# Performance work log

Hardware: AMD Instinct MI355X
Metric: run time of the kernel (lower is better)

Reference implementation:

```python
import jax, jax.numpy as jnp
import numpy as np

B, T, E = 4096, 200, 64
H1, H2 = 80, 40  # att_hidden_units


def setup_inputs() -> dict:
    key = jax.random.key(0)
    ks = jax.random.split(key, 9)
    glorot = jax.nn.initializers.glorot_normal()
    return {
        "queries": jax.random.normal(ks[0], (B, 1, E), jnp.float32),
        "keys": jax.random.normal(ks[1], (B, T, E), jnp.float32),
        "keys_length": jax.random.randint(ks[2], (B, 1), 0, T, jnp.int32),
        "W1": glorot(ks[3], (2 * E, H1), jnp.float32),
        "b1": jnp.zeros((H1,), jnp.float32),
        "W2": glorot(ks[4], (H1, H2), jnp.float32),
        "b2": jnp.zeros((H2,), jnp.float32),
        "kernel": glorot(ks[5], (H2, 1), jnp.float32),
        "bias": jnp.zeros((1,), jnp.float32),
    }


def reference(queries, keys, keys_length, W1, b1, W2, b2, kernel, bias):
    b, t, e = keys.shape
    # tile query across all T key positions and concat -> (B, T, 2E)
    q = jnp.broadcast_to(queries, (b, t, e))
    att_input = jnp.concatenate([q, keys], axis=-1)
    # local activation unit: small per-key MLP with sigmoid activations
    h = jax.nn.sigmoid(att_input @ W1 + b1)   # (B, T, H1)
    h = jax.nn.sigmoid(h @ W2 + b2)           # (B, T, H2)
    score = h @ kernel + bias                 # (B, T, 1)
    scores = jnp.transpose(score, (0, 2, 1))  # (B, 1, T)
    # sequence mask from keys_length (B, 1)
    mask = jnp.arange(t)[None, None, :] < keys_length[:, :, None]  # (B, 1, T)
    paddings = jnp.full_like(scores, -(2.0 ** 32) + 1.0)
    scores = jnp.where(mask, scores, paddings)
    # weight_normalization=True -> softmax over T
    weights = jax.nn.softmax(scores, axis=-1)  # (B, 1, T)
    # weighted-sum pooling over keys -> (B, 1, E)
    out = jnp.matmul(weights, keys)
    return out
```

## Files before the change

### kernel.cpp

```cpp
#include <hip/hip_runtime.h>
#include <hip/hip_bf16.h>

#define TT 200
#define EE 64

typedef unsigned short u16;
typedef unsigned int u32;
typedef __attribute__((ext_vector_type(8))) short bfrag;
typedef __attribute__((ext_vector_type(4))) float f32x4;

__device__ __forceinline__ u16 f2bf(float f) {
    __hip_bfloat16 h(f);
    return __builtin_bit_cast(u16, h);
}
__device__ __forceinline__ float bf2f(u16 h) {
    return __uint_as_float(((u32)h) << 16);
}
__device__ __forceinline__ float sigmoid_fast(float x) {
    return __builtin_amdgcn_rcpf(1.0f + __expf(-x));
}

__global__ void prep_frags(const float* __restrict__ W1, const float* __restrict__ W2,
                           u16* __restrict__ A1p, u16* __restrict__ A2p,
                           u16* __restrict__ A1q) {
    int idx = blockIdx.x * 256 + threadIdx.x;
    if (idx < 5 * 2 * 64 * 8) {
        int j = idx & 7, l = (idx >> 3) & 63, ks = (idx >> 9) & 1, mt5 = idx >> 10;
        int g = l >> 4, m = mt5 * 16 + (l & 15);
        int k = ks * 32 + g * 8 + j;
        A1p[idx] = f2bf(W1[(64 + k) * 80 + m]);
        A1q[idx] = f2bf(W1[k * 80 + m]);
    }
    if (idx < 3 * 3 * 64 * 8) {
        int j = idx & 7, l = (idx >> 3) & 63, ks = (idx >> 9) % 3, m2 = idx / 1536;
        int g = l >> 4, m = m2 * 16 + (l & 15);
        int i24 = ks * 8 + j;
        u16 v = 0;
        if (i24 < 20 && m < 40) {
            int mt5 = i24 >> 2, r = i24 & 3;
            int k = mt5 * 16 + g * 4 + r;
            v = f2bf(W2[k * 40 + m]);
        }
        A2p[idx] = v;
    }
}

#define LOADK32(MT, QA0, QA1, QA2, QA3, QB0, QB1, QB2, QB3) {           \
    int ra_ = (MT) * 32 + l15;                                          \
    QA0 = QA1 = QA2 = QA3 = make_float4(0.f, 0.f, 0.f, 0.f);            \
    QB0 = QB1 = QB2 = QB3 = make_float4(0.f, 0.f, 0.f, 0.f);            \
    if (ra_ < lenEff) {                                                 \
        const float* p_ = kb + ra_ * EE + g * 8;                        \
        QA0 = *reinterpret_cast<const float4*>(p_);                     \
        QA1 = *reinterpret_cast<const float4*>(p_ + 4);                 \
        QA2 = *reinterpret_cast<const float4*>(p_ + 32);                \
        QA3 = *reinterpret_cast<const float4*>(p_ + 36);                \
    }                                                                   \
    if (ra_ + 16 < lenEff) {                                            \
        const float* p_ = kb + (ra_ + 16) * EE + g * 8;                 \
        QB0 = *reinterpret_cast<const float4*>(p_);                     \
        QB1 = *reinterpret_cast<const float4*>(p_ + 4);                 \
        QB2 = *reinterpret_cast<const float4*>(p_ + 32);                \
        QB3 = *reinterpret_cast<const float4*>(p_ + 36);                \
    } }

#define PACK(A, X, Y) {                                                 \
    A[0] = (short)f2bf(X.x); A[1] = (short)f2bf(X.y);                   \
    A[2] = (short)f2bf(X.z); A[3] = (short)f2bf(X.w);                   \
    A[4] = (short)f2bf(Y.x); A[5] = (short)f2bf(Y.y);                   \
    A[6] = (short)f2bf(Y.z); A[7] = (short)f2bf(Y.w); }

__global__ __launch_bounds__(256, 2) void din_mfma(
    const float* __restrict__ queries,
    const float* __restrict__ keys,
    const int*   __restrict__ keys_length,
    const float* __restrict__ b1,
    const float* __restrict__ b2,
    const float* __restrict__ wk,
    const float* __restrict__ bias,
    const u16*   __restrict__ A1p,
    const u16*   __restrict__ A2p,
    const u16*   __restrict__ A1q,
    float* __restrict__ out)
{
    __shared__ __align__(16) u16 w1ls[5 * 2 * 64 * 8];
    __shared__ __align__(16) u16 w2ls[3 * 3 * 64 * 8];
    __shared__ __align__(16) float wkls[48];
    __shared__ __align__(16) float b2ls[48];
    __shared__ __align__(16) float qils[4][80];

    const int tid  = threadIdx.x;
    const int lane = tid & 63;
    const int wv   = tid >> 6;
    const int l15  = lane & 15;
    const int g    = lane >> 4;
    const int b    = blockIdx.x * 4 + wv;

    const float* kb = keys + (size_t)b * (TT * EE);
    const float* q  = queries + (size_t)b * EE;
    const int len   = keys_length[b];
    const float biass = bias[0];

    const int lenEff = (len == 0) ? TT : len;
    const int ntiles = (lenEff + 31) >> 5;

    float4 qa0, qa1, qa2, qa3, qb0, qb1_, qb2, qb3;
    LOADK32(0, qa0, qa1, qa2, qa3, qb0, qb1_, qb2, qb3);

    for (int c = tid; c < 640; c += 256)
        *reinterpret_cast<float4*>(&w1ls[c * 8]) = reinterpret_cast<const float4*>(A1p)[c];
    for (int c = tid; c < 576; c += 256)
        *reinterpret_cast<float4*>(&w2ls[c * 8]) = reinterpret_cast<const float4*>(A2p)[c];
    if (tid < 48) {
        wkls[tid] = (tid < 40) ? wk[tid] : 0.f;
        b2ls[tid] = (tid < 40) ? b2[tid] : 0.f;
    }

    {
        bfrag qf0, qf1;
        const float* qp = q + g * 8;
        float4 q0 = *reinterpret_cast<const float4*>(qp);
        float4 q1 = *reinterpret_cast<const float4*>(qp + 4);
        float4 q2 = *reinterpret_cast<const float4*>(qp + 32);
        float4 q3 = *reinterpret_cast<const float4*>(qp + 36);
        PACK(qf0, q0, q1); PACK(qf1, q2, q3);
        #pragma unroll
        for (int mt5 = 0; mt5 < 5; ++mt5) {
            bfrag aq0 = *reinterpret_cast<const bfrag*>(A1q + (((mt5 * 2 + 0) * 64 + lane) << 3));
            bfrag aq1 = *reinterpret_cast<const bfrag*>(A1q + (((mt5 * 2 + 1) * 64 + lane) << 3));
            f32x4 c = { 0.f, 0.f, 0.f, 0.f };
            c = __builtin_amdgcn_mfma_f32_16x16x32_bf16(aq0, qf0, c, 0, 0, 0);
            c = __builtin_amdgcn_mfma_f32_16x16x32_bf16(aq1, qf1, c, 0, 0, 0);
            float4 bv = *reinterpret_cast<const float4*>(b1 + mt5 * 16 + g * 4);
            if (l15 == 0) {
                float4 o = { c[0] + bv.x, c[1] + bv.y, c[2] + bv.z, c[3] + bv.w };
                *reinterpret_cast<float4*>(&qils[wv][mt5 * 16 + g * 4]) = o;
            }
        }
    }
    __syncthreads();

    float acc[16];
    #pragma unroll
    for (int j = 0; j < 16; ++j) acc[j] = 0.f;
    float Z = 0.f;

    bfrag a0, a1, a2, a3;
    PACK(a0, qa0, qa1); PACK(a1, qa2, qa3);
    PACK(a2, qb0, qb1_); PACK(a3, qb2, qb3);

    for (int mt = 0; mt < ntiles; ++mt) {
        if (mt + 1 < ntiles) { LOADK32(mt + 1, qa0, qa1, qa2, qa3, qb0, qb1_, qb2, qb3); }
        const bool hasB = (mt * 32 + 16) < lenEff;

        bfrag xa0, xa1, xa2;
        {
            f32x4 d[5];
            #pragma unroll
            for (int mt5 = 0; mt5 < 5; ++mt5) {
                bfrag wA = *reinterpret_cast<const bfrag*>(&w1ls[((mt5 * 2 + 0) * 64 + lane) * 8]);
                bfrag wB = *reinterpret_cast<const bfrag*>(&w1ls[((mt5 * 2 + 1) * 64 + lane) * 8]);
                f32x4 c = *reinterpret_cast<const f32x4*>(&qils[wv][mt5 * 16 + g * 4]);
                c = __builtin_amdgcn_mfma_f32_16x16x32_bf16(wA, a0, c, 0, 0, 0);
                c = __builtin_amdgcn_mfma_f32_16x16x32_bf16(wB, a1, c, 0, 0, 0);
                d[mt5] = c;
            }
            #pragma unroll
            for (int j = 0; j < 8; ++j) {
                xa0[j] = (short)f2bf(sigmoid_fast(d[j >> 2][j & 3]));
                xa1[j] = (short)f2bf(sigmoid_fast(d[(8 + j) >> 2][(8 + j) & 3]));
                xa2[j] = (short)((16 + j) < 20
                            ? f2bf(sigmoid_fast(d[(16 + j) >> 2][(16 + j) & 3])) : 0);
            }
        }

        float pa = 0.f, pb = 0.f, ea, eb;
        const int ra = mt * 32 + l15, rb = ra + 16;

        if (hasB) {
            bfrag xb0, xb1, xb2;
            {
                f32x4 d[5];
                #pragma unroll
                for (int mt5 = 0; mt5 < 5; ++mt5) {
                    bfrag wA = *reinterpret_cast<const bfrag*>(&w1ls[((mt5 * 2 + 0) * 64 + lane) * 8]);
                    bfrag wB = *reinterpret_cast<const bfrag*>(&w1ls[((mt5 * 2 + 1) * 64 + lane) * 8]);
                    f32x4 c = *reinterpret_cast<const f32x4*>(&qils[wv][mt5 * 16 + g * 4]);
                    c = __builtin_amdgcn_mfma_f32_16x16x32_bf16(wA, a2, c, 0, 0, 0);
                    c = __builtin_amdgcn_mfma_f32_16x16x32_bf16(wB, a3, c, 0, 0, 0);
                    d[mt5] = c;
                }
                #pragma unroll
                for (int j = 0; j < 8; ++j) {
                    xb0[j] = (short)f2bf(sigmoid_fast(d[j >> 2][j & 3]));
                    xb1[j] = (short)f2bf(sigmoid_fast(d[(8 + j) >> 2][(8 + j) & 3]));
                    xb2[j] = (short)((16 + j) < 20
                                ? f2bf(sigmoid_fast(d[(16 + j) >> 2][(16 + j) & 3])) : 0);
                }
            }
            #pragma unroll
            for (int m2 = 0; m2 < 3; ++m2) {
                bfrag u0 = *reinterpret_cast<const bfrag*>(&w2ls[((m2 * 3 + 0) * 64 + lane) * 8]);
                bfrag u1 = *reinterpret_cast<const bfrag*>(&w2ls[((m2 * 3 + 1) * 64 + lane) * 8]);
                bfrag u2 = *reinterpret_cast<const bfrag*>(&w2ls[((m2 * 3 + 2) * 64 + lane) * 8]);
                f32x4 ci = *reinterpret_cast<const f32x4*>(&b2ls[m2 * 16 + g * 4]);
                f32x4 wv4 = *reinterpret_cast<const f32x4*>(&wkls[m2 * 16 + g * 4]);
                f32x4 ca = ci, cb = ci;
                ca = __builtin_amdgcn_mfma_f32_16x16x32_bf16(u0, xa0, ca, 0, 0, 0);
                ca = __builtin_amdgcn_mfma_f32_16x16x32_bf16(u1, xa1, ca, 0, 0, 0);
                ca = __builtin_amdgcn_mfma_f32_16x16x32_bf16(u2, xa2, ca, 0, 0, 0);
                cb = __builtin_amdgcn_mfma_f32_16x16x32_bf16(u0, xb0, cb, 0, 0, 0);
                cb = __builtin_amdgcn_mfma_f32_16x16x32_bf16(u1, xb1, cb, 0, 0, 0);
                cb = __builtin_amdgcn_mfma_f32_16x16x32_bf16(u2, xb2, cb, 0, 0, 0);
                #pragma unroll
                for (int rr = 0; rr < 4; ++rr) {
                    pa = fmaf(sigmoid_fast(ca[rr]), wv4[rr], pa);
                    pb = fmaf(sigmoid_fast(cb[rr]), wv4[rr], pb);
                }
            }
            pa += __shfl_xor(pa, 16); pa += __shfl_xor(pa, 32);
            pb += __shfl_xor(pb, 16); pb += __shfl_xor(pb, 32);
            ea = (ra < len) ? __expf(pa + biass) : ((len == 0 && ra < TT) ? 1.f : 0.f);
            eb = (rb < len) ? __expf(pb + biass) : ((len == 0 && rb < TT) ? 1.f : 0.f);
            Z += ea + eb;
            #pragma unroll
            for (int j = 0; j < 8; ++j) {
                acc[j]     = fmaf(ea, bf2f((u16)a0[j]), fmaf(eb, bf2f((u16)a2[j]), acc[j]));
                acc[8 + j] = fmaf(ea, bf2f((u16)a1[j]), fmaf(eb, bf2f((u16)a3[j]), acc[8 + j]));
            }
        } else {
            #pragma unroll
            for (int m2 = 0; m2 < 3; ++m2) {
                bfrag u0 = *reinterpret_cast<const bfrag*>(&w2ls[((m2 * 3 + 0) * 64 + lane) * 8]);
                bfrag u1 = *reinterpret_cast<const bfrag*>(&w2ls[((m2 * 3 + 1) * 64 + lane) * 8]);
                bfrag u2 = *reinterpret_cast<const bfrag*>(&w2ls[((m2 * 3 + 2) * 64 + lane) * 8]);
                f32x4 ci = *reinterpret_cast<const f32x4*>(&b2ls[m2 * 16 + g * 4]);
                f32x4 wv4 = *reinterpret_cast<const f32x4*>(&wkls[m2 * 16 + g * 4]);
                f32x4 ca = ci;
                ca = __builtin_amdgcn_mfma_f32_16x16x32_bf16(u0, xa0, ca, 0, 0, 0);
                ca = __builtin_amdgcn_mfma_f32_16x16x32_bf16(u1, xa1, ca, 0, 0, 0);
                ca = __builtin_amdgcn_mfma_f32_16x16x32_bf16(u2, xa2, ca, 0, 0, 0);
                #pragma unroll
                for (int rr = 0; rr < 4; ++rr)
                    pa = fmaf(sigmoid_fast(ca[rr]), wv4[rr], pa);
            }
            pa += __shfl_xor(pa, 16); pa += __shfl_xor(pa, 32);
            ea = (ra < len) ? __expf(pa + biass) : ((len == 0 && ra < TT) ? 1.f : 0.f);
            Z += ea;
            #pragma unroll
            for (int j = 0; j < 8; ++j) {
                acc[j]     = fmaf(ea, bf2f((u16)a0[j]), acc[j]);
                acc[8 + j] = fmaf(ea, bf2f((u16)a1[j]), acc[8 + j]);
            }
        }

        if (mt + 1 < ntiles) {
            PACK(a0, qa0, qa1); PACK(a1, qa2, qa3);
            PACK(a2, qb0, qb1_); PACK(a3, qb2, qb3);
        }
    }

    Z += __shfl_xor(Z, 1); Z += __shfl_xor(Z, 2);
    Z += __shfl_xor(Z, 4); Z += __shfl_xor(Z, 8);
    #pragma unroll
    for (int j = 0; j < 16; ++j) {
        acc[j] += __shfl_xor(acc[j], 1);
        acc[j] += __shfl_xor(acc[j], 2);
        acc[j] += __shfl_xor(acc[j], 4);
        acc[j] += __shfl_xor(acc[j], 8);
    }
    if (l15 == 0) {
        float inv = __builtin_amdgcn_rcpf(Z);
        float* ob = out + (size_t)b * EE + g * 8;
        float4 o0 = { acc[0] * inv,  acc[1] * inv,  acc[2] * inv,  acc[3] * inv };
        float4 o1 = { acc[4] * inv,  acc[5] * inv,  acc[6] * inv,  acc[7] * inv };
        float4 o2 = { acc[8] * inv,  acc[9] * inv,  acc[10] * inv, acc[11] * inv };
        float4 o3 = { acc[12] * inv, acc[13] * inv, acc[14] * inv, acc[15] * inv };
        *reinterpret_cast<float4*>(ob)      = o0;
        *reinterpret_cast<float4*>(ob + 4)  = o1;
        *reinterpret_cast<float4*>(ob + 32) = o2;
        *reinterpret_cast<float4*>(ob + 36) = o3;
    }
}

extern "C" void kernel_launch(void* const* d_in, const int* in_sizes, int n_in,
                              void* d_out, int out_size, void* d_ws, size_t ws_size,
                              hipStream_t stream) {
    const float* queries = (const float*)d_in[0];
    const float* keys    = (const float*)d_in[1];
    const int*   klen    = (const int*)d_in[2];
    const float* W1      = (const float*)d_in[3];
    const float* b1      = (const float*)d_in[4];
    const float* W2      = (const float*)d_in[5];
    const float* b2      = (const float*)d_in[6];
    const float* wk      = (const float*)d_in[7];
    const float* bias    = (const float*)d_in[8];
    float* out           = (float*)d_out;

    u16* A1p = (u16*)d_ws;
    u16* A2p = (u16*)((char*)d_ws + 10240);
    u16* A1q = (u16*)((char*)d_ws + 19456);

    prep_frags<<<20, 256, 0, stream>>>(W1, W2, A1p, A2p, A1q);
    din_mfma<<<1024, 256, 0, stream>>>(queries, keys, klen, b1, b2, wk, bias,
                                       A1p, A2p, A1q, out);
}
```

Before: 51.66 us.

## Load-balance key tiles across the block's waves with an LDS work queue

Instead of each wave processing one batch row's tiles, all four waves in a block pull 32-row tiles from a shared atomic counter covering the block's four rows. Partial softmax numerators and denominators are written to LDS per wave and reduced at the end. This targets the imbalance caused by variable keys_length, where waves with short rows sit idle while one wave handles a long row. The cost is an LDS atomic per tile, extra LDS for the reduction buffers and a final block-wide sync. Because the shared exponentials are not max-subtracted, summing partials across waves is still exact.

```diff
diff --git a/kernel.cpp b/kernel.cpp
--- a/kernel.cpp
+++ b/kernel.cpp
@@ -45,23 +45,23 @@
     }
 }
 
-#define LOADK32(MT, QA0, QA1, QA2, QA3, QB0, QB1, QB2, QB3) {           \
-    int ra_ = (MT) * 32 + l15;                                          \
-    QA0 = QA1 = QA2 = QA3 = make_float4(0.f, 0.f, 0.f, 0.f);            \
-    QB0 = QB1 = QB2 = QB3 = make_float4(0.f, 0.f, 0.f, 0.f);            \
-    if (ra_ < lenEff) {                                                 \
-        const float* p_ = kb + ra_ * EE + g * 8;                        \
-        QA0 = *reinterpret_cast<const float4*>(p_);                     \
-        QA1 = *reinterpret_cast<const float4*>(p_ + 4);                 \
-        QA2 = *reinterpret_cast<const float4*>(p_ + 32);                \
-        QA3 = *reinterpret_cast<const float4*>(p_ + 36);                \
-    }                                                                   \
-    if (ra_ + 16 < lenEff) {                                            \
-        const float* p_ = kb + (ra_ + 16) * EE + g * 8;                 \
-        QB0 = *reinterpret_cast<const float4*>(p_);                     \
-        QB1 = *reinterpret_cast<const float4*>(p_ + 4);                 \
-        QB2 = *reinterpret_cast<const float4*>(p_ + 32);                \
-        QB3 = *reinterpret_cast<const float4*>(p_ + 36);                \
+#define LOADK32D(KB, MT, LEF, QA0, QA1, QA2, QA3, QB0, QB1, QB2, QB3) {  \
+    int ra_ = (MT) * 32 + l15;                                           \
+    QA0 = QA1 = QA2 = QA3 = make_float4(0.f, 0.f, 0.f, 0.f);             \
+    QB0 = QB1 = QB2 = QB3 = make_float4(0.f, 0.f, 0.f, 0.f);             \
+    if (ra_ < (LEF)) {                                                   \
+        const float* p_ = (KB) + ra_ * EE + g * 8;                       \
+        QA0 = *reinterpret_cast<const float4*>(p_);                      \
+        QA1 = *reinterpret_cast<const float4*>(p_ + 4);                  \
+        QA2 = *reinterpret_cast<const float4*>(p_ + 32);                 \
+        QA3 = *reinterpret_cast<const float4*>(p_ + 36);                 \
+    }                                                                    \
+    if (ra_ + 16 < (LEF)) {                                              \
+        const float* p_ = (KB) + (ra_ + 16) * EE + g * 8;                \
+        QB0 = *reinterpret_cast<const float4*>(p_);                      \
+        QB1 = *reinterpret_cast<const float4*>(p_ + 4);                  \
+        QB2 = *reinterpret_cast<const float4*>(p_ + 32);                 \
+        QB3 = *reinterpret_cast<const float4*>(p_ + 36);                 \
     } }
 
 #define PACK(A, X, Y) {                                                 \
@@ -88,24 +88,26 @@
     __shared__ __align__(16) float wkls[48];
     __shared__ __align__(16) float b2ls[48];
     __shared__ __align__(16) float qils[4][80];
+    __shared__ __align__(16) float redls[4][4][64];
+    __shared__ float zls[4][4];
+    __shared__ int ntls[4], lenls[4];
+    __shared__ u32 qh;
 
     const int tid  = threadIdx.x;
     const int lane = tid & 63;
     const int wv   = tid >> 6;
     const int l15  = lane & 15;
     const int g    = lane >> 4;
-    const int b    = blockIdx.x * 4 + wv;
-
-    const float* kb = keys + (size_t)b * (TT * EE);
-    const float* q  = queries + (size_t)b * EE;
-    const int len   = keys_length[b];
+    const int bbase = blockIdx.x * 4;
+    const int b    = bbase + wv;
     const float biass = bias[0];
 
-    const int lenEff = (len == 0) ? TT : len;
-    const int ntiles = (lenEff + 31) >> 5;
-
-    float4 qa0, qa1, qa2, qa3, qb0, qb1_, qb2, qb3;
-    LOADK32(0, qa0, qa1, qa2, qa3, qb0, qb1_, qb2, qb3);
+    const int len0 = keys_length[b];
+    const int lef0 = (len0 == 0) ? TT : len0;
+    if (lane == 0) { ntls[wv] = (lef0 + 31) >> 5; lenls[wv] = len0; }
+    if (tid == 0) qh = 0;
+    for (int c = tid; c < 1024; c += 256) (&redls[0][0][0])[c] = 0.f;
+    if (tid < 16) (&zls[0][0])[tid] = 0.f;
 
     for (int c = tid; c < 640; c += 256)
         *reinterpret_cast<float4*>(&w1ls[c * 8]) = reinterpret_cast<const float4*>(A1p)[c];
@@ -118,7 +120,7 @@
 
     {
         bfrag qf0, qf1;
-        const float* qp = q + g * 8;
+        const float* qp = queries + (size_t)b * EE + g * 8;
         float4 q0 = *reinterpret_cast<const float4*>(qp);
         float4 q1 = *reinterpret_cast<const float4*>(qp + 4);
         float4 q2 = *reinterpret_cast<const float4*>(qp + 32);
@@ -140,18 +142,47 @@
     }
     __syncthreads();
 
+    const int nt0 = ntls[0], nt1 = ntls[1], nt2 = ntls[2], nt3 = ntls[3];
+    const int c1 = nt0, c2 = nt0 + nt1, c3 = nt0 + nt1 + nt2, total = c3 + nt3;
+
     float acc[16];
     #pragma unroll
     for (int j = 0; j < 16; ++j) acc[j] = 0.f;
     float Z = 0.f;
 
+    int icur;
+    if (lane == 0) icur = (int)atomicAdd(&qh, 1u);
+    icur = __shfl(icur, 0);
+
+    int blc = 0, mtc = 0, lenc = 0, lefc = 0;
     bfrag a0, a1, a2, a3;
-    PACK(a0, qa0, qa1); PACK(a1, qa2, qa3);
-    PACK(a2, qb0, qb1_); PACK(a3, qb2, qb3);
-
-    for (int mt = 0; mt < ntiles; ++mt) {
-        if (mt + 1 < ntiles) { LOADK32(mt + 1, qa0, qa1, qa2, qa3, qb0, qb1_, qb2, qb3); }
-        const bool hasB = (mt * 32 + 16) < lenEff;
+    if (icur < total) {
+        blc = (icur >= c1) + (icur >= c2) + (icur >= c3);
+        mtc = icur - (blc == 0 ? 0 : (blc == 1 ? c1 : (blc == 2 ? c2 : c3)));
+        lenc = lenls[blc]; lefc = (lenc == 0) ? TT : lenc;
+        const float* kbp = keys + (size_t)(bbase + blc) * (TT * EE);
+        float4 t0, t1, t2, t3, t4, t5, t6, t7;
+        LOADK32D(kbp, mtc, lefc, t0, t1, t2, t3, t4, t5, t6, t7);
+        PACK(a0, t0, t1); PACK(a1, t2, t3);
+        PACK(a2, t4, t5); PACK(a3, t6, t7);
+    }
+
+    while (icur < total) {
+        int inext;
+        if (lane == 0) inext = (int)atomicAdd(&qh, 1u);
+        inext = __shfl(inext, 0);
+        int bln = 0, mtn = 0, lenn = 0, lefn = 0;
+        float4 n0, n1, n2, n3, n4, n5, n6, n7;
+        n0 = n1 = n2 = n3 = n4 = n5 = n6 = n7 = make_float4(0.f, 0.f, 0.f, 0.f);
+        if (inext < total) {
+            bln = (inext >= c1) + (inext >= c2) + (inext >= c3);
+            mtn = inext - (bln == 0 ? 0 : (bln == 1 ? c1 : (bln == 2 ? c2 : c3)));
+            lenn = lenls[bln]; lefn = (lenn == 0) ? TT : lenn;
+            const float* kbp = keys + (size_t)(bbase + bln) * (TT * EE);
+            LOADK32D(kbp, mtn, lefn, n0, n1, n2, n3, n4, n5, n6, n7);
+        }
+
+        const bool hasB = (mtc * 32 + 16) < lefc;
 
         bfrag xa0, xa1, xa2;
         {
@@ -160,7 +191,7 @@
             for (int mt5 = 0; mt5 < 5; ++mt5) {
                 bfrag wA = *reinterpret_cast<const bfrag*>(&w1ls[((mt5 * 2 + 0) * 64 + lane) * 8]);
                 bfrag wB = *reinterpret_cast<const bfrag*>(&w1ls[((mt5 * 2 + 1) * 64 + lane) * 8]);
-                f32x4 c = *reinterpret_cast<const f32x4*>(&qils[wv][mt5 * 16 + g * 4]);
+                f32x4 c = *reinterpret_cast<const f32x4*>(&qils[blc][mt5 * 16 + g * 4]);
                 c = __builtin_amdgcn_mfma_f32_16x16x32_bf16(wA, a0, c, 0, 0, 0);
                 c = __builtin_amdgcn_mfma_f32_16x16x32_bf16(wB, a1, c, 0, 0, 0);
                 d[mt5] = c;
@@ -175,7 +206,7 @@
         }
 
         float pa = 0.f, pb = 0.f, ea, eb;
-        const int ra = mt * 32 + l15, rb = ra + 16;
+        const int ra = mtc * 32 + l15, rb = ra + 16;
 
         if (hasB) {
             bfrag xb0, xb1, xb2;
@@ -185,7 +216,7 @@
                 for (int mt5 = 0; mt5 < 5; ++mt5) {
                     bfrag wA = *reinterpret_cast<const bfrag*>(&w1ls[((mt5 * 2 + 0) * 64 + lane) * 8]);
                     bfrag wB = *reinterpret_cast<const bfrag*>(&w1ls[((mt5 * 2 + 1) * 64 + lane) * 8]);
-                    f32x4 c = *reinterpret_cast<const f32x4*>(&qils[wv][mt5 * 16 + g * 4]);
+                    f32x4 c = *reinterpret_cast<const f32x4*>(&qils[blc][mt5 * 16 + g * 4]);
                     c = __builtin_amdgcn_mfma_f32_16x16x32_bf16(wA, a2, c, 0, 0, 0);
                     c = __builtin_amdgcn_mfma_f32_16x16x32_bf16(wB, a3, c, 0, 0, 0);
                     d[mt5] = c;
@@ -220,8 +251,8 @@
             }
             pa += __shfl_xor(pa, 16); pa += __shfl_xor(pa, 32);
             pb += __shfl_xor(pb, 16); pb += __shfl_xor(pb, 32);
-            ea = (ra < len) ? __expf(pa + biass) : ((len == 0 && ra < TT) ? 1.f : 0.f);
-            eb = (rb < len) ? __expf(pb + biass) : ((len == 0 && rb < TT) ? 1.f : 0.f);
+            ea = (ra < lenc) ? __expf(pa + biass) : ((lenc == 0 && ra < TT) ? 1.f : 0.f);
+            eb = (rb < lenc) ? __expf(pb + biass) : ((lenc == 0 && rb < TT) ? 1.f : 0.f);
             Z += ea + eb;
             #pragma unroll
             for (int j = 0; j < 8; ++j) {
@@ -245,7 +276,7 @@
                     pa = fmaf(sigmoid_fast(ca[rr]), wv4[rr], pa);
             }
             pa += __shfl_xor(pa, 16); pa += __shfl_xor(pa, 32);
-            ea = (ra < len) ? __expf(pa + biass) : ((len == 0 && ra < TT) ? 1.f : 0.f);
+            ea = (ra < lenc) ? __expf(pa + biass) : ((lenc == 0 && ra < TT) ? 1.f : 0.f);
             Z += ea;
             #pragma unroll
             for (int j = 0; j < 8; ++j) {
@@ -254,32 +285,43 @@
             }
         }
 
-        if (mt + 1 < ntiles) {
-            PACK(a0, qa0, qa1); PACK(a1, qa2, qa3);
-            PACK(a2, qb0, qb1_); PACK(a3, qb2, qb3);
-        }
-    }
-
-    Z += __shfl_xor(Z, 1); Z += __shfl_xor(Z, 2);
-    Z += __shfl_xor(Z, 4); Z += __shfl_xor(Z, 8);
-    #pragma unroll
-    for (int j = 0; j < 16; ++j) {
-        acc[j] += __shfl_xor(acc[j], 1);
-        acc[j] += __shfl_xor(acc[j], 2);
-        acc[j] += __shfl_xor(acc[j], 4);
-        acc[j] += __shfl_xor(acc[j], 8);
-    }
-    if (l15 == 0) {
-        float inv = __builtin_amdgcn_rcpf(Z);
-        float* ob = out + (size_t)b * EE + g * 8;
-        float4 o0 = { acc[0] * inv,  acc[1] * inv,  acc[2] * inv,  acc[3] * inv };
-        float4 o1 = { acc[4] * inv,  acc[5] * inv,  acc[6] * inv,  acc[7] * inv };
-        float4 o2 = { acc[8] * inv,  acc[9] * inv,  acc[10] * inv, acc[11] * inv };
-        float4 o3 = { acc[12] * inv, acc[13] * inv, acc[14] * inv, acc[15] * inv };
-        *reinterpret_cast<float4*>(ob)      = o0;
-        *reinterpret_cast<float4*>(ob + 4)  = o1;
-        *reinterpret_cast<float4*>(ob + 32) = o2;
-        *reinterpret_cast<float4*>(ob + 36) = o3;
+        if (inext >= total || bln != blc) {
+            Z += __shfl_xor(Z, 1); Z += __shfl_xor(Z, 2);
+            Z += __shfl_xor(Z, 4); Z += __shfl_xor(Z, 8);
+            #pragma unroll
+            for (int j = 0; j < 16; ++j) {
+                acc[j] += __shfl_xor(acc[j], 1);
+                acc[j] += __shfl_xor(acc[j], 2);
+                acc[j] += __shfl_xor(acc[j], 4);
+                acc[j] += __shfl_xor(acc[j], 8);
+            }
+            if (l15 == 0) {
+                #pragma unroll
+                for (int j = 0; j < 8; ++j) {
+                    redls[blc][wv][g * 8 + j]      = acc[j];
+                    redls[blc][wv][32 + g * 8 + j] = acc[8 + j];
+                }
+                if (lane == 0) zls[blc][wv] = Z;
+            }
+            #pragma unroll
+            for (int j = 0; j < 16; ++j) acc[j] = 0.f;
+            Z = 0.f;
+        }
+
+        if (inext < total) {
+            PACK(a0, n0, n1); PACK(a1, n2, n3);
+            PACK(a2, n4, n5); PACK(a3, n6, n7);
+        }
+        icur = inext; blc = bln; mtc = mtn; lenc = lenn; lefc = lefn;
+    }
+    __syncthreads();
+
+    {
+        const int bat = tid >> 6, feat = tid & 63;
+        float s = (redls[bat][0][feat] + redls[bat][1][feat])
+                + (redls[bat][2][feat] + redls[bat][3][feat]);
+        float Zt = (zls[bat][0] + zls[bat][1]) + (zls[bat][2] + zls[bat][3]);
+        out[(size_t)(bbase + bat) * EE + feat] = s * __builtin_amdgcn_rcpf(Zt);
     }
 }
 
```

New measurement: 56.98 us. +10.3%, slower.
